# Optimization experiments

Measured on AMD Instinct MI355X. Metric: run time of the kernel, lower is better.

The kernel has to match this reference:

```python
import jax, jax.numpy as jnp
import numpy as np

BN_EPS = 1e-5

def _bn_relu(x, gamma, beta):
    # training-mode BatchNorm1d: biased batch stats over (B, N) per channel
    mean = x.mean(axis=(0, 2), keepdims=True)
    var = x.var(axis=(0, 2), keepdims=True)
    xn = (x - mean) * jax.lax.rsqrt(var + BN_EPS)
    return jax.nn.relu(xn * gamma[None, :, None] + beta[None, :, None])


def setup_inputs() -> dict:
    key = jax.random.key(0)
    ks = jax.random.split(key, 12)
    B, n1, n2, c1, c2 = 16, 4096, 1024, 128, 256
    in_ch, mlp = c1 + c2, [256, 128]
    xyz1 = jax.random.uniform(ks[0], (B, n1, 3), dtype=jnp.float32)
    xyz2 = jax.random.uniform(ks[1], (B, n2, 3), dtype=jnp.float32)
    feat1 = jax.random.normal(ks[2], (B, c1, n1), dtype=jnp.float32)
    feat2 = jax.random.normal(ks[3], (B, c2, n2), dtype=jnp.float32)
    # Conv1d(k=1) weights as (out, in) matrices; kaiming-ish scale
    w0 = jax.random.normal(ks[4], (mlp[0], in_ch), dtype=jnp.float32) / np.sqrt(in_ch)
    b0 = jnp.zeros((mlp[0],), jnp.float32)
    g0 = jnp.ones((mlp[0],), jnp.float32)
    be0 = jnp.zeros((mlp[0],), jnp.float32)
    w1 = jax.random.normal(ks[5], (mlp[1], mlp[0]), dtype=jnp.float32) / np.sqrt(mlp[0])
    b1 = jnp.zeros((mlp[1],), jnp.float32)
    g1 = jnp.ones((mlp[1],), jnp.float32)
    be1 = jnp.zeros((mlp[1],), jnp.float32)
    return {"xyz1": xyz1, "xyz2": xyz2, "feat1": feat1, "feat2": feat2,
            "w0": w0, "b0": b0, "g0": g0, "be0": be0,
            "w1": w1, "b1": b1, "g1": g1, "be1": be1}


def reference(xyz1, xyz2, feat1, feat2, w0, b0, g0, be0, w1, b1, g1, be1):
    # three_nn_interpolate: squared pairwise dists (B, n1, n2)
    d = jnp.sum((xyz1[:, :, None, :] - xyz2[:, None, :, :]) ** 2, axis=-1)
    neg_d3, idx3 = jax.lax.top_k(-d, 3)          # 3 smallest dists
    d3 = -neg_d3                                  # (B, n1, 3)
    w = 1.0 / (d3 + 1e-8)
    w = w / jnp.sum(w, axis=-1, keepdims=True)
    # gather feat2 at knn indices: (B, c2, n1, 3)
    gathered = jnp.take_along_axis(feat2[:, :, None, :], idx3[:, None, :, :], axis=3)
    interp = jnp.sum(gathered * w[:, None, :, :], axis=-1)  # (B, c2, n1)

    x = jnp.concatenate([feat1, interp], axis=1)            # (B, c1+c2, n1)
    x = _bn_relu(jnp.einsum('oc,bcn->bon', w0, x) + b0[None, :, None], g0, be0)
    x = _bn_relu(jnp.einsum('oc,bcn->bon', w1, x) + b1[None, :, None], g1, be1)
    return x
```

## Files before the change

### kernel.cpp

```cpp
#include <hip/hip_runtime.h>
#include <hip/hip_bf16.h>

typedef unsigned short u16;
typedef __attribute__((ext_vector_type(8))) __bf16 bf16x8;
typedef __attribute__((ext_vector_type(4))) float floatx4;

#define B_   16
#define N1_  4096
#define N2_  1024
#define C1_  128
#define C2_  256
#define CIN_ 384
#define CM_  256
#define CO_  128

__device__ __forceinline__ u16 f2bf(float f) {
  unsigned u = __float_as_uint(f);
  u = (u + 0x7fffu + ((u >> 16) & 1u)) >> 16;
  return (u16)u;
}
__device__ __forceinline__ float bf2f(u16 h) {
  return __uint_as_float(((unsigned)h) << 16);
}

union U128 { uint4 u; bf16x8 v; u16 s[8]; };

__device__ __forceinline__ bf16x8 ldfrag(const u16* p) {
  U128 x; x.u = *(const uint4*)p; return x.v;
}
__device__ __forceinline__ uint4 pack8(const u16* h) {
  uint4 u;
  u.x = (unsigned)h[0] | ((unsigned)h[1] << 16);
  u.y = (unsigned)h[2] | ((unsigned)h[3] << 16);
  u.z = (unsigned)h[4] | ((unsigned)h[5] << 16);
  u.w = (unsigned)h[6] | ((unsigned)h[7] << 16);
  return u;
}


__global__ __launch_bounds__(256) void knn_part_kernel(
    const float* __restrict__ xyz1, const float* __restrict__ xyz2,
    float* __restrict__ pd, int* __restrict__ pi,
    const float* __restrict__ w0, const float* __restrict__ w1,
    u16* __restrict__ w0b, u16* __restrict__ w1b)
{
  __shared__ float4 sp[128];
  int t = threadIdx.x;
  if (blockIdx.x == 16) {
    int item = (blockIdx.y * 8 + blockIdx.z) * 256 + t;
    if (item < 12288) {
      int m = item / 48, kc = item % 48;
      const float* p = w0 + m * CIN_ + kc * 8;
      u16 h8[8];
      #pragma unroll
      for (int j = 0; j < 8; ++j) h8[j] = f2bf(p[j]);
      int mt = m >> 4, col = m & 15, kt = kc >> 2, quad = kc & 3;
      *(uint4*)(w0b + ((mt*12 + kt)*512 + (quad*16 + col)*8)) = pack8(h8);
    } else if (item < 16384) {
      int i2 = item - 12288;
      int m = i2 >> 5, kc = i2 & 31;
      const float* p = w1 + m * CM_ + kc * 8;
      u16 h8[8];
      #pragma unroll
      for (int j = 0; j < 8; ++j) h8[j] = f2bf(p[j]);
      int mt = m >> 4, col = m & 15, kt = kc >> 2, quad = kc & 3;
      *(uint4*)(w1b + ((mt*8 + kt)*512 + (quad*16 + col)*8)) = pack8(h8);
    }
    return;
  }
  int b = blockIdx.y, chunk = blockIdx.z;
  const float* p2 = xyz2 + ((size_t)b * N2_ + chunk * 128) * 3;
  if (t < 128) sp[t] = make_float4(p2[t*3], p2[t*3+1], p2[t*3+2], 0.f);
  __syncthreads();
  int i = blockIdx.x * 256 + t;
  const float* p1 = xyz1 + ((size_t)b * N1_ + i) * 3;
  float x = p1[0], y = p1[1], z = p1[2];
  float d0 = 1e30f, d1 = 1e30f, d2 = 1e30f;
  int i0 = 0, i1 = 0, i2 = 0;
  int jb = chunk * 128;
  #pragma unroll 4
  for (int j = 0; j < 128; ++j) {
    float4 p = sp[j];
    float dx = x - p.x, dy = y - p.y, dz = z - p.z;
    float d = dx*dx + dy*dy + dz*dz;
    if (d < d2) {
      int jj = jb + j;
      if (d < d0)      { d2=d1; i2=i1; d1=d0; i1=i0; d0=d; i0=jj; }
      else if (d < d1) { d2=d1; i2=i1; d1=d;  i1=jj; }
      else             { d2=d;  i2=jj; }
    }
  }
  int o = chunk*65536 + b*4096 + i;
  pd[o] = d0; pd[o + 524288] = d1; pd[o + 1048576] = d2;
  pi[o] = i0; pi[o + 524288] = i1; pi[o + 1048576] = i2;
}

__global__ __launch_bounds__(256) void tr2m_kernel(
    const float* __restrict__ feat2, u16* __restrict__ feat2Tb,
    const float* __restrict__ pd, const int* __restrict__ pi,
    int* __restrict__ idx_out, float* __restrict__ w_out)
{
  __shared__ float sA[64][257];
  int t = threadIdx.x;
  if (blockIdx.x >= 16) {
    int p = (blockIdx.y * 16 + (blockIdx.x - 16)) * 256 + t;
    float d0 = 1e30f, d1 = 1e30f, d2 = 1e30f;
    int i0 = 0, i1 = 0, i2 = 0;
    #pragma unroll
    for (int c = 0; c < 8; ++c) {
      int o = c*65536 + p;
      #pragma unroll
      for (int k = 0; k < 3; ++k) {
        float d = pd[o + k*524288];
        int ix = pi[o + k*524288];
        bool c2 = d < d2, c1 = d < d1, c0 = d < d0;
        d2 = c1 ? d1 : (c2 ? d  : d2);
        i2 = c1 ? i1 : (c2 ? ix : i2);
        d1 = c0 ? d0 : (c1 ? d  : d1);
        i1 = c0 ? i0 : (c1 ? ix : i1);
        d0 = c0 ? d  : d0;
        i0 = c0 ? ix : i0;
      }
    }
    float w0 = 1.f/(d0+1e-8f), w1 = 1.f/(d1+1e-8f), w2 = 1.f/(d2+1e-8f);
    float inv = 1.f/(w0+w1+w2);
    idx_out[p]          = i0;
    idx_out[p +  65536] = i1;
    idx_out[p + 131072] = i2;
    w_out[p]            = w0*inv;
    w_out[p +  65536]   = w1*inv;
    w_out[p + 131072]   = w2*inv;
    return;
  }
  int b = blockIdx.y;
  int n0 = blockIdx.x * 64;
  #pragma unroll
  for (int j = 0; j < 16; ++j) {
    int flat4 = t + j * 256;
    int c = flat4 >> 4, nn4 = (flat4 & 15) * 4;
    float4 v = *(const float4*)(feat2 + ((size_t)b*C2_ + c)*N2_ + n0 + nn4);
    sA[nn4+0][c] = v.x; sA[nn4+1][c] = v.y; sA[nn4+2][c] = v.z; sA[nn4+3][c] = v.w;
  }
  __syncthreads();
  int nn = t & 63, chunk = t >> 6;
  u16* dst = feat2Tb + ((size_t)b*N2_ + n0 + nn)*C2_ + chunk*64;
  #pragma unroll
  for (int g = 0; g < 8; ++g) {
    u16 h8[8];
    #pragma unroll
    for (int j = 0; j < 8; ++j) h8[j] = f2bf(sA[nn][chunk*64 + g*8 + j]);
    *(uint4*)(dst + g*8) = pack8(h8);
  }
}

__global__ __launch_bounds__(256) void prep_fused_kernel(
    const float* __restrict__ feat1, const u16* __restrict__ feat2Tb,
    const int* __restrict__ idx_in, const float* __restrict__ w_in,
    u16* __restrict__ xcatT)
{
  __shared__ float sA[64][133];
  int b = blockIdx.y;
  int t = threadIdx.x;
  if (blockIdx.x < 64) {
    int n0 = blockIdx.x * 64;
    #pragma unroll
    for (int j = 0; j < 8; ++j) {
      int flat4 = t + j * 256;
      int c = flat4 >> 4, nn4 = (flat4 & 15) * 4;
      float4 v = *(const float4*)(feat1 + ((size_t)b*C1_ + c)*N1_ + n0 + nn4);
      sA[nn4+0][c] = v.x; sA[nn4+1][c] = v.y; sA[nn4+2][c] = v.z; sA[nn4+3][c] = v.w;
    }
    __syncthreads();
    int nn = t & 63, chunk = t >> 6;
    int n = n0 + nn, nt = n >> 4, col = n & 15;
    u16* tb = xcatT + ((size_t)b*256 + nt)*12*512;
    #pragma unroll
    for (int g = 0; g < 4; ++g) {
      int c0 = chunk*32 + g*8;
      u16 h8[8];
      #pragma unroll
      for (int j = 0; j < 8; ++j) h8[j] = f2bf(sA[nn][c0 + j]);
      *(uint4*)(tb + (size_t)chunk*512 + (g*16 + col)*8) = pack8(h8);
    }
  } else {
    int p0 = (blockIdx.x - 64) * 64;
    int seg = t & 31;
    int pl  = t >> 5;
    #pragma unroll 2
    for (int pass = 0; pass < 8; ++pass) {
      int n = p0 + pass*8 + pl;
      int base = b*N1_ + n;
      int i0 = idx_in[base], i1 = idx_in[base + 65536], i2 = idx_in[base + 131072];
      float w0 = w_in[base], w1 = w_in[base + 65536], w2 = w_in[base + 131072];
      const u16* fb = feat2Tb + (size_t)b*N2_*C2_ + seg*8;
      U128 a, c, d;
      a.u = *(const uint4*)(fb + (size_t)i0*C2_);
      c.u = *(const uint4*)(fb + (size_t)i1*C2_);
      d.u = *(const uint4*)(fb + (size_t)i2*C2_);
      u16 h8[8];
      #pragma unroll
      for (int j = 0; j < 8; ++j)
        h8[j] = f2bf(w0*bf2f(a.s[j]) + w1*bf2f(c.s[j]) + w2*bf2f(d.s[j]));
      int nt = n >> 4, col = n & 15;
      int kt = 4 + (seg >> 2), quad = seg & 3;
      *(uint4*)(xcatT + (((size_t)b*256 + nt)*12 + kt)*512 + (quad*16 + col)*8) = pack8(h8);
    }
  }
}

__global__ __launch_bounds__(256) void gemm1_mfma(
    const u16* __restrict__ xcatT, const u16* __restrict__ w0b,
    const float* __restrict__ b0p, u16* __restrict__ y0T,
    float* __restrict__ p0)
{
  __shared__ u16 sbuf[2][16][512];
  __shared__ float ps[4][64][2];
  int t = threadIdx.x;
  int wave = t >> 6, lane = t & 63;
  int col = lane & 15, quad = lane >> 4;
  int wm = wave >> 1, wn = wave & 1;
  int b = blockIdx.y;
  int mtb8 = blockIdx.z * 8;
  int ntb8 = blockIdx.x * 8;

  const u16* asrc = w0b + (size_t)mtb8 * 12 * 512 + lane * 8;
  const u16* bsrc = xcatT + ((size_t)(b * 256 + ntb8) * 12) * 512 + lane * 8;
  const u16* stage_base = (wave < 2) ? (asrc + (size_t)(wave * 4) * 12 * 512)
                                     : (bsrc + (size_t)((wave - 2) * 4) * 12 * 512);

  floatx4 acc[4][4] = {};

  #pragma unroll
  for (int i = 0; i < 4; ++i)
    __builtin_amdgcn_global_load_lds(
        (const __attribute__((address_space(1))) void*)(stage_base + (size_t)i * 12 * 512),
        (__attribute__((address_space(3))) void*)(&sbuf[0][wave * 4 + i][0]),
        16, 0, 0);
  __syncthreads();

  int cur = 0;
  #pragma unroll 1
  for (int kt = 0; kt < 12; ++kt) {
    if (kt < 11) {
      #pragma unroll
      for (int i = 0; i < 4; ++i)
        __builtin_amdgcn_global_load_lds(
            (const __attribute__((address_space(1))) void*)(stage_base + (size_t)(i * 12 + kt + 1) * 512),
            (__attribute__((address_space(3))) void*)(&sbuf[cur ^ 1][wave * 4 + i][0]),
            16, 0, 0);
    }
    bf16x8 af[4], bfr[4];
    #pragma unroll
    for (int i = 0; i < 4; ++i) {
      af[i]  = ldfrag(&sbuf[cur][wm * 4 + i][lane * 8]);
      bfr[i] = ldfrag(&sbuf[cur][8 + wn * 4 + i][lane * 8]);
    }
    #pragma unroll
    for (int mt = 0; mt < 4; ++mt)
      #pragma unroll
      for (int nt = 0; nt < 4; ++nt)
        acc[mt][nt] = __builtin_amdgcn_mfma_f32_16x16x32_bf16(af[mt], bfr[nt], acc[mt][nt], 0, 0, 0);
    __syncthreads();
    cur ^= 1;
  }

  int m0 = blockIdx.z*128 + wm*64;
  #pragma unroll
  for (int mt = 0; mt < 4; ++mt) {
    float4 bias4 = *(const float4*)(b0p + m0 + mt*16 + quad*4);
    float bia[4] = {bias4.x, bias4.y, bias4.z, bias4.w};
    int kt_out = (m0 >> 5) + (mt >> 1);
    int quad_out = ((mt & 1) << 1) | (quad >> 1);
    int j0 = (quad & 1) * 4;
    float s[4] = {}, q[4] = {};
    int ntb = ntb8 + wn*4;
    #pragma unroll
    for (int nt = 0; nt < 4; ++nt) {
      int nt_g = ntb + nt;
      u16 h[4];
      #pragma unroll
      for (int r = 0; r < 4; ++r) {
        float v = acc[mt][nt][r] + bia[r];
        u16 hh = f2bf(v);
        float vr = bf2f(hh);
        h[r] = hh; s[r] += vr; q[r] += vr*vr;
      }
      *(ushort4*)(y0T + (((size_t)b*256 + nt_g)*8 + kt_out)*512 + (quad_out*16 + col)*8 + j0)
          = make_ushort4(h[0], h[1], h[2], h[3]);
    }
    #pragma unroll
    for (int r = 0; r < 4; ++r) {
      float ss = s[r], qq = q[r];
      #pragma unroll
      for (int msk = 1; msk < 16; msk <<= 1) { ss += __shfl_xor(ss, msk); qq += __shfl_xor(qq, msk); }
      if (col == 0) {
        ps[wave][mt*16 + quad*4 + r][0] = ss;
        ps[wave][mt*16 + quad*4 + r][1] = qq;
      }
    }
  }
  __syncthreads();
  {
    int c = t >> 1, k = t & 1;
    int wbase = (c >> 6) * 2, ch = c & 63;
    float v = ps[wbase][ch][k] + ps[wbase+1][ch][k];
    size_t l = (size_t)blockIdx.z*512 + blockIdx.y*32 + blockIdx.x;
    p0[l*256 + t] = v;
  }
}

__global__ __launch_bounds__(256) void stats_kernel(
    const float* __restrict__ p, const float* __restrict__ g,
    const float* __restrict__ be, float* __restrict__ scale,
    float* __restrict__ shift, int half_split, int nl)
{
  int c = blockIdx.x, t = threadIdx.x;
  size_t base = half_split ? ((size_t)(c >> 7) * 512 * 256 + (size_t)(c & 127) * 2)
                           : ((size_t)c * 2);
  float s = 0.f, q = 0.f;
  for (int i = 0; i < nl; ++i) {
    float2 v = *(const float2*)(p + base + (size_t)(t + i*256) * 256);
    s += v.x; q += v.y;
  }
  #pragma unroll
  for (int m = 1; m < 64; m <<= 1) { s += __shfl_xor(s, m); q += __shfl_xor(q, m); }
  __shared__ float2 red[4];
  if ((t & 63) == 0) red[t >> 6] = make_float2(s, q);
  __syncthreads();
  if (t == 0) {
    float ss = red[0].x + red[1].x + red[2].x + red[3].x;
    float qq = red[0].y + red[1].y + red[2].y + red[3].y;
    float mu  = ss * (1.f/65536.f);
    float var = qq * (1.f/65536.f) - mu*mu;
    float a = g[c] * rsqrtf(var + 1e-5f);
    scale[c] = a; shift[c] = be[c] - mu*a;
  }
}

__global__ __launch_bounds__(256) void gemm2_mfma(
    const u16* __restrict__ y0T, const u16* __restrict__ w1b,
    const float* __restrict__ b1p,
    const float* __restrict__ scale0, const float* __restrict__ shift0,
    float* __restrict__ out, float* __restrict__ p1)
{
  __shared__ u16 sbuf[2][12][512];
  __shared__ float a0s[CM_], bb0s[CM_];
  __shared__ float ps[4][64][2];
  int t = threadIdx.x;
  a0s[t] = scale0[t]; bb0s[t] = shift0[t];
  int wave = t >> 6, lane = t & 63;
  int col = lane & 15, quad = lane >> 4;
  int wm = wave >> 1, wn = wave & 1;
  int b = blockIdx.y;
  int ntb4 = blockIdx.x * 4;

  const u16* src[3];
  #pragma unroll
  for (int i = 0; i < 3; ++i) {
    int f = wave * 3 + i;
    src[i] = (f < 8) ? (w1b + (size_t)(f * 8) * 512 + lane * 8)
                     : (y0T + ((size_t)(b * 256 + ntb4 + (f - 8)) * 8) * 512 + lane * 8);
  }

  floatx4 acc[4][2] = {};

  #pragma unroll
  for (int i = 0; i < 3; ++i)
    __builtin_amdgcn_global_load_lds(
        (const __attribute__((address_space(1))) void*)(src[i]),
        (__attribute__((address_space(3))) void*)(&sbuf[0][wave * 3 + i][0]),
        16, 0, 0);
  __syncthreads();

  int cur = 0;
  #pragma unroll 1
  for (int kt = 0; kt < 8; ++kt) {
    if (kt < 7) {
      #pragma unroll
      for (int i = 0; i < 3; ++i)
        __builtin_amdgcn_global_load_lds(
            (const __attribute__((address_space(1))) void*)(src[i] + (size_t)(kt + 1) * 512),
            (__attribute__((address_space(3))) void*)(&sbuf[cur ^ 1][wave * 3 + i][0]),
            16, 0, 0);
    }
    bf16x8 af[4]; U128 braw[2];
    #pragma unroll
    for (int i = 0; i < 4; ++i) af[i] = ldfrag(&sbuf[cur][wm * 4 + i][lane * 8]);
    #pragma unroll
    for (int j = 0; j < 2; ++j) braw[j].u = *(const uint4*)(&sbuf[cur][8 + wn * 2 + j][lane * 8]);
    int c0 = kt * 32 + quad * 8;
    float av[8], bv[8];
    *(float4*)&av[0] = *(const float4*)&a0s[c0];  *(float4*)&av[4] = *(const float4*)&a0s[c0+4];
    *(float4*)&bv[0] = *(const float4*)&bb0s[c0]; *(float4*)&bv[4] = *(const float4*)&bb0s[c0+4];
    bf16x8 bfv[2];
    #pragma unroll
    for (int j = 0; j < 2; ++j) {
      u16 h8[8];
      #pragma unroll
      for (int e = 0; e < 8; ++e)
        h8[e] = f2bf(fmaxf(fmaf(bf2f(braw[j].s[e]), av[e], bv[e]), 0.f));
      U128 x; x.u = pack8(h8); bfv[j] = x.v;
    }
    #pragma unroll
    for (int mt = 0; mt < 4; ++mt)
      #pragma unroll
      for (int nt = 0; nt < 2; ++nt)
        acc[mt][nt] = __builtin_amdgcn_mfma_f32_16x16x32_bf16(af[mt], bfv[nt], acc[mt][nt], 0, 0, 0);
    __syncthreads();
    cur ^= 1;
  }

  int m0 = wm * 64;
  int n0 = blockIdx.x * 64 + wn * 32;
  #pragma unroll
  for (int mt = 0; mt < 4; ++mt) {
    float4 bias4 = *(const float4*)(b1p + m0 + mt*16 + quad*4);
    float bia[4] = {bias4.x, bias4.y, bias4.z, bias4.w};
    float s[4] = {}, q[4] = {};
    #pragma unroll
    for (int nt = 0; nt < 2; ++nt) {
      int n = n0 + nt*16 + col;
      #pragma unroll
      for (int r = 0; r < 4; ++r) {
        float v = acc[mt][nt][r] + bia[r];
        out[((size_t)b*CO_ + m0 + mt*16 + quad*4 + r)*N1_ + n] = v;
        s[r] += v; q[r] += v*v;
      }
    }
    #pragma unroll
    for (int r = 0; r < 4; ++r) {
      float ss = s[r], qq = q[r];
      #pragma unroll
      for (int msk = 1; msk < 16; msk <<= 1) { ss += __shfl_xor(ss, msk); qq += __shfl_xor(qq, msk); }
      if (col == 0) {
        ps[wave][mt*16 + quad*4 + r][0] = ss;
        ps[wave][mt*16 + quad*4 + r][1] = qq;
      }
    }
  }
  __syncthreads();
  {
    int c = t >> 1, k = t & 1;
    int wbase = (c >> 6) * 2, ch = c & 63;
    float v = ps[wbase][ch][k] + ps[wbase+1][ch][k];
    size_t l = (size_t)blockIdx.y*64 + blockIdx.x;
    p1[l*256 + t] = v;
  }
}

__global__ __launch_bounds__(256) void bnrelu_kernel(
    float* __restrict__ out, const float* __restrict__ scale1, const float* __restrict__ shift1)
{
  int idx = blockIdx.x * 256 + threadIdx.x;
  int c = (idx >> 10) & (CO_ - 1);
  float a = scale1[c];
  float bb = shift1[c];
  float4 v = ((const float4*)out)[idx];
  v.x = fmaxf(fmaf(v.x, a, bb), 0.f);
  v.y = fmaxf(fmaf(v.y, a, bb), 0.f);
  v.z = fmaxf(fmaf(v.z, a, bb), 0.f);
  v.w = fmaxf(fmaf(v.w, a, bb), 0.f);
  ((float4*)out)[idx] = v;
}

extern "C" void kernel_launch(void* const* d_in, const int* in_sizes, int n_in,
                              void* d_out, int out_size, void* d_ws, size_t ws_size,
                              hipStream_t stream)
{
  const float* xyz1  = (const float*)d_in[0];
  const float* xyz2  = (const float*)d_in[1];
  const float* feat1 = (const float*)d_in[2];
  const float* feat2 = (const float*)d_in[3];
  const float* w0    = (const float*)d_in[4];
  const float* b0    = (const float*)d_in[5];
  const float* g0    = (const float*)d_in[6];
  const float* be0   = (const float*)d_in[7];
  const float* w1    = (const float*)d_in[8];
  const float* b1    = (const float*)d_in[9];
  const float* g1    = (const float*)d_in[10];
  const float* be1   = (const float*)d_in[11];
  float* out = (float*)d_out;
  char* ws = (char*)d_ws;

  u16*   xcatT   = (u16*)ws;
  float* knn_pd  = (float*)ws;
  float* p1      = (float*)ws;
  int*   knn_pi  = (int*)(ws + 6291456);
  u16*   y0T     = (u16*)(ws + 50331648);
  u16*   feat2Tb = (u16*)(ws + 50331648);
  u16*   w0b     = (u16*)(ws + 83886080);
  u16*   w1b     = (u16*)(ws + 84082688);
  int*   idx_buf = (int*)(ws + 84148224);
  float* w_buf   = (float*)(ws + 84934656);
  float* p0      = (float*)(ws + 85721088);
  float* scale0  = (float*)(ws + 87293952);
  float* shift0  = scale0 + 256;
  float* scale1  = scale0 + 512;
  float* shift1  = scale0 + 640;

  knn_part_kernel <<<dim3(17,16,8),   256, 0, stream>>>(xyz1, xyz2, knn_pd, knn_pi, w0, w1, w0b, w1b);
  tr2m_kernel     <<<dim3(32,16),     256, 0, stream>>>(feat2, feat2Tb, knn_pd, knn_pi, idx_buf, w_buf);
  prep_fused_kernel<<<dim3(128,16),   256, 0, stream>>>(feat1, feat2Tb, idx_buf, w_buf, xcatT);
  gemm1_mfma      <<<dim3(32,16,2),   256, 0, stream>>>(xcatT, w0b, b0, y0T, p0);
  stats_kernel    <<<256,             256, 0, stream>>>(p0, g0, be0, scale0, shift0, 1, 2);
  gemm2_mfma      <<<dim3(64,16),     256, 0, stream>>>(y0T, w1b, b1, scale0, shift0, out, p1);
  stats_kernel    <<<128,             256, 0, stream>>>(p1, g1, be1, scale1, shift1, 0, 4);
  bnrelu_kernel   <<<8192,            256, 0, stream>>>(out, scale1, shift1);
}
```

Before: 244.4 us.

## Use single-wave GEMM blocks with 128x64 tiles and channel-major stat partials

Both GEMM kernels drop from four-wave 256-thread blocks to single-wave 64-thread blocks. Each wave now computes an 8x4 grid of MFMA tiles and stages all A and B fragments itself, with no cross-wave LDS partial reduction. Per-block BN partial sums are written channel-major, so the stats kernel reads contiguous float2 values. This trades block-level cooperation for more independent blocks and higher per-wave register use. That may lower occupancy, and each wave now issues 12 global-to-LDS loads per k-step.

```diff
diff --git a/kernel.cpp b/kernel.cpp
--- a/kernel.cpp
+++ b/kernel.cpp
@@ -208,34 +208,33 @@
   }
 }
 
-__global__ __launch_bounds__(256) void gemm1_mfma(
+__global__ __launch_bounds__(64) void gemm1_mfma(
     const u16* __restrict__ xcatT, const u16* __restrict__ w0b,
     const float* __restrict__ b0p, u16* __restrict__ y0T,
     float* __restrict__ p0)
 {
-  __shared__ u16 sbuf[2][16][512];
-  __shared__ float ps[4][64][2];
-  int t = threadIdx.x;
-  int wave = t >> 6, lane = t & 63;
+  __shared__ u16 sbuf[2][12][512];
+  int lane = threadIdx.x;
   int col = lane & 15, quad = lane >> 4;
-  int wm = wave >> 1, wn = wave & 1;
-  int b = blockIdx.y;
-  int mtb8 = blockIdx.z * 8;
-  int ntb8 = blockIdx.x * 8;
-
-  const u16* asrc = w0b + (size_t)mtb8 * 12 * 512 + lane * 8;
-  const u16* bsrc = xcatT + ((size_t)(b * 256 + ntb8) * 12) * 512 + lane * 8;
-  const u16* stage_base = (wave < 2) ? (asrc + (size_t)(wave * 4) * 12 * 512)
-                                     : (bsrc + (size_t)((wave - 2) * 4) * 12 * 512);
-
-  floatx4 acc[4][4] = {};
-
-  #pragma unroll
-  for (int i = 0; i < 4; ++i)
+  int mb = blockIdx.x;
+  int gnb = blockIdx.y;
+  int b = gnb >> 6;
+  int ntb4 = (gnb & 63) * 4;
+
+  const u16* src[12];
+  #pragma unroll
+  for (int i = 0; i < 12; ++i)
+    src[i] = (i < 8)
+      ? (w0b + (size_t)((mb*8 + i) * 12) * 512 + lane*8)
+      : (xcatT + (size_t)((b*256 + ntb4 + (i-8)) * 12) * 512 + lane*8);
+
+  floatx4 acc[8][4] = {};
+
+  #pragma unroll
+  for (int i = 0; i < 12; ++i)
     __builtin_amdgcn_global_load_lds(
-        (const __attribute__((address_space(1))) void*)(stage_base + (size_t)i * 12 * 512),
-        (__attribute__((address_space(3))) void*)(&sbuf[0][wave * 4 + i][0]),
-        16, 0, 0);
+        (const __attribute__((address_space(1))) void*)(src[i]),
+        (__attribute__((address_space(3))) void*)(&sbuf[0][i][0]), 16, 0, 0);
   __syncthreads();
 
   int cur = 0;
@@ -243,20 +242,18 @@
   for (int kt = 0; kt < 12; ++kt) {
     if (kt < 11) {
       #pragma unroll
-      for (int i = 0; i < 4; ++i)
+      for (int i = 0; i < 12; ++i)
         __builtin_amdgcn_global_load_lds(
-            (const __attribute__((address_space(1))) void*)(stage_base + (size_t)(i * 12 + kt + 1) * 512),
-            (__attribute__((address_space(3))) void*)(&sbuf[cur ^ 1][wave * 4 + i][0]),
-            16, 0, 0);
-    }
-    bf16x8 af[4], bfr[4];
-    #pragma unroll
-    for (int i = 0; i < 4; ++i) {
-      af[i]  = ldfrag(&sbuf[cur][wm * 4 + i][lane * 8]);
-      bfr[i] = ldfrag(&sbuf[cur][8 + wn * 4 + i][lane * 8]);
-    }
-    #pragma unroll
-    for (int mt = 0; mt < 4; ++mt)
+            (const __attribute__((address_space(1))) void*)(src[i] + (size_t)(kt+1)*512),
+            (__attribute__((address_space(3))) void*)(&sbuf[cur^1][i][0]), 16, 0, 0);
+    }
+    bf16x8 af[8], bfr[4];
+    #pragma unroll
+    for (int i = 0; i < 8; ++i) af[i] = ldfrag(&sbuf[cur][i][lane*8]);
+    #pragma unroll
+    for (int j = 0; j < 4; ++j) bfr[j] = ldfrag(&sbuf[cur][8 + j][lane*8]);
+    #pragma unroll
+    for (int mt = 0; mt < 8; ++mt)
       #pragma unroll
       for (int nt = 0; nt < 4; ++nt)
         acc[mt][nt] = __builtin_amdgcn_mfma_f32_16x16x32_bf16(af[mt], bfr[nt], acc[mt][nt], 0, 0, 0);
@@ -264,19 +261,17 @@
     cur ^= 1;
   }
 
-  int m0 = blockIdx.z*128 + wm*64;
-  #pragma unroll
-  for (int mt = 0; mt < 4; ++mt) {
+  int m0 = mb * 128;
+  #pragma unroll
+  for (int mt = 0; mt < 8; ++mt) {
     float4 bias4 = *(const float4*)(b0p + m0 + mt*16 + quad*4);
     float bia[4] = {bias4.x, bias4.y, bias4.z, bias4.w};
-    int kt_out = (m0 >> 5) + (mt >> 1);
+    int kt_out = mb*4 + (mt >> 1);
     int quad_out = ((mt & 1) << 1) | (quad >> 1);
     int j0 = (quad & 1) * 4;
     float s[4] = {}, q[4] = {};
-    int ntb = ntb8 + wn*4;
     #pragma unroll
     for (int nt = 0; nt < 4; ++nt) {
-      int nt_g = ntb + nt;
       u16 h[4];
       #pragma unroll
       for (int r = 0; r < 4; ++r) {
@@ -285,7 +280,7 @@
         float vr = bf2f(hh);
         h[r] = hh; s[r] += vr; q[r] += vr*vr;
       }
-      *(ushort4*)(y0T + (((size_t)b*256 + nt_g)*8 + kt_out)*512 + (quad_out*16 + col)*8 + j0)
+      *(ushort4*)(y0T + (((size_t)b*256 + ntb4 + nt)*8 + kt_out)*512 + (quad_out*16 + col)*8 + j0)
           = make_ushort4(h[0], h[1], h[2], h[3]);
     }
     #pragma unroll
@@ -293,33 +288,24 @@
       float ss = s[r], qq = q[r];
       #pragma unroll
       for (int msk = 1; msk < 16; msk <<= 1) { ss += __shfl_xor(ss, msk); qq += __shfl_xor(qq, msk); }
-      if (col == 0) {
-        ps[wave][mt*16 + quad*4 + r][0] = ss;
-        ps[wave][mt*16 + quad*4 + r][1] = qq;
-      }
-    }
-  }
-  __syncthreads();
-  {
-    int c = t >> 1, k = t & 1;
-    int wbase = (c >> 6) * 2, ch = c & 63;
-    float v = ps[wbase][ch][k] + ps[wbase+1][ch][k];
-    size_t l = (size_t)blockIdx.z*512 + blockIdx.y*32 + blockIdx.x;
-    p0[l*256 + t] = v;
+      if (col == 0)
+        *(float2*)(p0 + ((size_t)(mb*128 + mt*16 + quad*4 + r) * 1024 + gnb) * 2)
+            = make_float2(ss, qq);
+    }
   }
 }
 
 __global__ __launch_bounds__(256) void stats_kernel(
     const float* __restrict__ p, const float* __restrict__ g,
     const float* __restrict__ be, float* __restrict__ scale,
-    float* __restrict__ shift, int half_split, int nl)
+    float* __restrict__ shift)
 {
   int c = blockIdx.x, t = threadIdx.x;
-  size_t base = half_split ? ((size_t)(c >> 7) * 512 * 256 + (size_t)(c & 127) * 2)
-                           : ((size_t)c * 2);
+  const float* base = p + (size_t)c * 2048;
   float s = 0.f, q = 0.f;
-  for (int i = 0; i < nl; ++i) {
-    float2 v = *(const float2*)(p + base + (size_t)(t + i*256) * 256);
+  #pragma unroll
+  for (int i = 0; i < 4; ++i) {
+    float2 v = *(const float2*)(base + (size_t)(t + i*256) * 2);
     s += v.x; q += v.y;
   }
   #pragma unroll
@@ -337,7 +323,7 @@
   }
 }
 
-__global__ __launch_bounds__(256) void gemm2_mfma(
+__global__ __launch_bounds__(64) void gemm2_mfma(
     const u16* __restrict__ y0T, const u16* __restrict__ w1b,
     const float* __restrict__ b1p,
     const float* __restrict__ scale0, const float* __restrict__ shift0,
@@ -345,31 +331,29 @@
 {
   __shared__ u16 sbuf[2][12][512];
   __shared__ float a0s[CM_], bb0s[CM_];
-  __shared__ float ps[4][64][2];
-  int t = threadIdx.x;
-  a0s[t] = scale0[t]; bb0s[t] = shift0[t];
-  int wave = t >> 6, lane = t & 63;
+  int lane = threadIdx.x;
   int col = lane & 15, quad = lane >> 4;
-  int wm = wave >> 1, wn = wave & 1;
-  int b = blockIdx.y;
-  int ntb4 = blockIdx.x * 4;
-
-  const u16* src[3];
-  #pragma unroll
-  for (int i = 0; i < 3; ++i) {
-    int f = wave * 3 + i;
-    src[i] = (f < 8) ? (w1b + (size_t)(f * 8) * 512 + lane * 8)
-                     : (y0T + ((size_t)(b * 256 + ntb4 + (f - 8)) * 8) * 512 + lane * 8);
-  }
-
-  floatx4 acc[4][2] = {};
-
-  #pragma unroll
-  for (int i = 0; i < 3; ++i)
+  int gnb = blockIdx.x;
+  int b = gnb >> 6;
+  int ntb4 = (gnb & 63) * 4;
+
+  *(float4*)&a0s[lane*4]  = *(const float4*)(scale0 + lane*4);
+  *(float4*)&bb0s[lane*4] = *(const float4*)(shift0 + lane*4);
+
+  const u16* src[12];
+  #pragma unroll
+  for (int i = 0; i < 12; ++i)
+    src[i] = (i < 8)
+      ? (w1b + (size_t)(i * 8) * 512 + lane*8)
+      : (y0T + (size_t)((b*256 + ntb4 + (i-8)) * 8) * 512 + lane*8);
+
+  floatx4 acc[8][4] = {};
+
+  #pragma unroll
+  for (int i = 0; i < 12; ++i)
     __builtin_amdgcn_global_load_lds(
         (const __attribute__((address_space(1))) void*)(src[i]),
-        (__attribute__((address_space(3))) void*)(&sbuf[0][wave * 3 + i][0]),
-        16, 0, 0);
+        (__attribute__((address_space(3))) void*)(&sbuf[0][i][0]), 16, 0, 0);
   __syncthreads();
 
   int cur = 0;
@@ -377,24 +361,23 @@
   for (int kt = 0; kt < 8; ++kt) {
     if (kt < 7) {
       #pragma unroll
-      for (int i = 0; i < 3; ++i)
+      for (int i = 0; i < 12; ++i)
         __builtin_amdgcn_global_load_lds(
-            (const __attribute__((address_space(1))) void*)(src[i] + (size_t)(kt + 1) * 512),
-            (__attribute__((address_space(3))) void*)(&sbuf[cur ^ 1][wave * 3 + i][0]),
-            16, 0, 0);
-    }
-    bf16x8 af[4]; U128 braw[2];
-    #pragma unroll
-    for (int i = 0; i < 4; ++i) af[i] = ldfrag(&sbuf[cur][wm * 4 + i][lane * 8]);
-    #pragma unroll
-    for (int j = 0; j < 2; ++j) braw[j].u = *(const uint4*)(&sbuf[cur][8 + wn * 2 + j][lane * 8]);
-    int c0 = kt * 32 + quad * 8;
+            (const __attribute__((address_space(1))) void*)(src[i] + (size_t)(kt+1)*512),
+            (__attribute__((address_space(3))) void*)(&sbuf[cur^1][i][0]), 16, 0, 0);
+    }
+    bf16x8 af[8]; U128 braw[4];
+    #pragma unroll
+    for (int i = 0; i < 8; ++i) af[i] = ldfrag(&sbuf[cur][i][lane*8]);
+    #pragma unroll
+    for (int j = 0; j < 4; ++j) braw[j].u = *(const uint4*)(&sbuf[cur][8 + j][lane*8]);
+    int c0 = kt*32 + quad*8;
     float av[8], bv[8];
     *(float4*)&av[0] = *(const float4*)&a0s[c0];  *(float4*)&av[4] = *(const float4*)&a0s[c0+4];
     *(float4*)&bv[0] = *(const float4*)&bb0s[c0]; *(float4*)&bv[4] = *(const float4*)&bb0s[c0+4];
-    bf16x8 bfv[2];
-    #pragma unroll
-    for (int j = 0; j < 2; ++j) {
+    bf16x8 bfv[4];
+    #pragma unroll
+    for (int j = 0; j < 4; ++j) {
       u16 h8[8];
       #pragma unroll
       for (int e = 0; e < 8; ++e)
@@ -402,28 +385,26 @@
       U128 x; x.u = pack8(h8); bfv[j] = x.v;
     }
     #pragma unroll
-    for (int mt = 0; mt < 4; ++mt)
-      #pragma unroll
-      for (int nt = 0; nt < 2; ++nt)
+    for (int mt = 0; mt < 8; ++mt)
+      #pragma unroll
+      for (int nt = 0; nt < 4; ++nt)
         acc[mt][nt] = __builtin_amdgcn_mfma_f32_16x16x32_bf16(af[mt], bfv[nt], acc[mt][nt], 0, 0, 0);
     __syncthreads();
     cur ^= 1;
   }
 
-  int m0 = wm * 64;
-  int n0 = blockIdx.x * 64 + wn * 32;
-  #pragma unroll
-  for (int mt = 0; mt < 4; ++mt) {
-    float4 bias4 = *(const float4*)(b1p + m0 + mt*16 + quad*4);
+  #pragma unroll
+  for (int mt = 0; mt < 8; ++mt) {
+    float4 bias4 = *(const float4*)(b1p + mt*16 + quad*4);
     float bia[4] = {bias4.x, bias4.y, bias4.z, bias4.w};
     float s[4] = {}, q[4] = {};
     #pragma unroll
-    for (int nt = 0; nt < 2; ++nt) {
-      int n = n0 + nt*16 + col;
+    for (int nt = 0; nt < 4; ++nt) {
+      int n = ntb4*16 + nt*16 + col;
       #pragma unroll
       for (int r = 0; r < 4; ++r) {
         float v = acc[mt][nt][r] + bia[r];
-        out[((size_t)b*CO_ + m0 + mt*16 + quad*4 + r)*N1_ + n] = v;
+        out[((size_t)b*CO_ + mt*16 + quad*4 + r)*N1_ + n] = v;
         s[r] += v; q[r] += v*v;
       }
     }
@@ -432,19 +413,10 @@
       float ss = s[r], qq = q[r];
       #pragma unroll
       for (int msk = 1; msk < 16; msk <<= 1) { ss += __shfl_xor(ss, msk); qq += __shfl_xor(qq, msk); }
-      if (col == 0) {
-        ps[wave][mt*16 + quad*4 + r][0] = ss;
-        ps[wave][mt*16 + quad*4 + r][1] = qq;
-      }
-    }
-  }
-  __syncthreads();
-  {
-    int c = t >> 1, k = t & 1;
-    int wbase = (c >> 6) * 2, ch = c & 63;
-    float v = ps[wbase][ch][k] + ps[wbase+1][ch][k];
-    size_t l = (size_t)blockIdx.y*64 + blockIdx.x;
-    p1[l*256 + t] = v;
+      if (col == 0)
+        *(float2*)(p1 + ((size_t)(mt*16 + quad*4 + r) * 1024 + gnb) * 2)
+            = make_float2(ss, qq);
+    }
   }
 }
 
@@ -492,7 +464,7 @@
   u16*   w1b     = (u16*)(ws + 84082688);
   int*   idx_buf = (int*)(ws + 84148224);
   float* w_buf   = (float*)(ws + 84934656);
-  float* p0      = (float*)(ws + 85721088);
+  float* p0      = (float*)(ws + 84148224);
   float* scale0  = (float*)(ws + 87293952);
   float* shift0  = scale0 + 256;
   float* scale1  = scale0 + 512;
@@ -501,9 +473,9 @@
   knn_part_kernel <<<dim3(17,16,8),   256, 0, stream>>>(xyz1, xyz2, knn_pd, knn_pi, w0, w1, w0b, w1b);
   tr2m_kernel     <<<dim3(32,16),     256, 0, stream>>>(feat2, feat2Tb, knn_pd, knn_pi, idx_buf, w_buf);
   prep_fused_kernel<<<dim3(128,16),   256, 0, stream>>>(feat1, feat2Tb, idx_buf, w_buf, xcatT);
-  gemm1_mfma      <<<dim3(32,16,2),   256, 0, stream>>>(xcatT, w0b, b0, y0T, p0);
-  stats_kernel    <<<256,             256, 0, stream>>>(p0, g0, be0, scale0, shift0, 1, 2);
-  gemm2_mfma      <<<dim3(64,16),     256, 0, stream>>>(y0T, w1b, b1, scale0, shift0, out, p1);
-  stats_kernel    <<<128,             256, 0, stream>>>(p1, g1, be1, scale1, shift1, 0, 4);
+  gemm1_mfma      <<<dim3(2,1024),     64, 0, stream>>>(xcatT, w0b, b0, y0T, p0);
+  stats_kernel    <<<256,             256, 0, stream>>>(p0, g0, be0, scale0, shift0);
+  gemm2_mfma      <<<1024,             64, 0, stream>>>(y0T, w1b, b1, scale0, shift0, out, p1);
+  stats_kernel    <<<128,             256, 0, stream>>>(p1, g1, be1, scale1, shift1);
   bnrelu_kernel   <<<8192,            256, 0, stream>>>(out, scale1, shift1);
 }
```

Result: slower. 256.5 us (+4.9%).

## Load GEMM fragments directly from global into registers with triple-buffered prefetch

Applied to the files above, without the earlier changes.

Both MFMA GEMM kernels drop the LDS double buffer filled by global_load_lds and the per-iteration barriers. Each wave now loads its own A and B fragments straight from global memory into registers, rotating three register buffers so loads run ahead of the MFMAs. gemm2 also doubles its N tile per block (half the grid) and adjusts the partial-stats indexing and stats_kernel argument to match. The cost is duplicated global or L2 traffic, since waves no longer share staged tiles, and higher register pressure.

```diff
diff --git a/kernel.cpp b/kernel.cpp
--- a/kernel.cpp
+++ b/kernel.cpp
@@ -213,56 +213,44 @@
     const float* __restrict__ b0p, u16* __restrict__ y0T,
     float* __restrict__ p0)
 {
-  __shared__ u16 sbuf[2][16][512];
   __shared__ float ps[4][64][2];
   int t = threadIdx.x;
   int wave = t >> 6, lane = t & 63;
   int col = lane & 15, quad = lane >> 4;
   int wm = wave >> 1, wn = wave & 1;
   int b = blockIdx.y;
-  int mtb8 = blockIdx.z * 8;
-  int ntb8 = blockIdx.x * 8;
-
-  const u16* asrc = w0b + (size_t)mtb8 * 12 * 512 + lane * 8;
-  const u16* bsrc = xcatT + ((size_t)(b * 256 + ntb8) * 12) * 512 + lane * 8;
-  const u16* stage_base = (wave < 2) ? (asrc + (size_t)(wave * 4) * 12 * 512)
-                                     : (bsrc + (size_t)((wave - 2) * 4) * 12 * 512);
+  int mtb = blockIdx.z*8 + wm*4;
+  int ntb = blockIdx.x*8 + wn*4;
+
+  const u16* ap = w0b + lane*8;
+  const u16* bp = xcatT + ((size_t)(b*256 + ntb)*12)*512 + lane*8;
 
   floatx4 acc[4][4] = {};
-
-  #pragma unroll
-  for (int i = 0; i < 4; ++i)
-    __builtin_amdgcn_global_load_lds(
-        (const __attribute__((address_space(1))) void*)(stage_base + (size_t)i * 12 * 512),
-        (__attribute__((address_space(3))) void*)(&sbuf[0][wave * 4 + i][0]),
-        16, 0, 0);
-  __syncthreads();
-
-  int cur = 0;
-  #pragma unroll 1
-  for (int kt = 0; kt < 12; ++kt) {
-    if (kt < 11) {
-      #pragma unroll
-      for (int i = 0; i < 4; ++i)
-        __builtin_amdgcn_global_load_lds(
-            (const __attribute__((address_space(1))) void*)(stage_base + (size_t)(i * 12 + kt + 1) * 512),
-            (__attribute__((address_space(3))) void*)(&sbuf[cur ^ 1][wave * 4 + i][0]),
-            16, 0, 0);
-    }
-    bf16x8 af[4], bfr[4];
-    #pragma unroll
-    for (int i = 0; i < 4; ++i) {
-      af[i]  = ldfrag(&sbuf[cur][wm * 4 + i][lane * 8]);
-      bfr[i] = ldfrag(&sbuf[cur][8 + wn * 4 + i][lane * 8]);
-    }
-    #pragma unroll
-    for (int mt = 0; mt < 4; ++mt)
-      #pragma unroll
-      for (int nt = 0; nt < 4; ++nt)
-        acc[mt][nt] = __builtin_amdgcn_mfma_f32_16x16x32_bf16(af[mt], bfr[nt], acc[mt][nt], 0, 0, 0);
-    __syncthreads();
-    cur ^= 1;
-  }
+  bf16x8 aA[4], aB[4], aC[4], bA[4], bB[4], bC[4];
+
+#define G1_LDA(BUF, KT) { _Pragma("unroll") for (int i = 0; i < 4; ++i) \
+    BUF[i] = ldfrag(ap + (size_t)((mtb+i)*12 + (KT))*512); }
+#define G1_LDB(BUF, KT) { _Pragma("unroll") for (int i = 0; i < 4; ++i) \
+    BUF[i] = ldfrag(bp + (size_t)(i*12 + (KT))*512); }
+#define G1_MM(A_, B_) { _Pragma("unroll") for (int mt = 0; mt < 4; ++mt) \
+    _Pragma("unroll") for (int nt = 0; nt < 4; ++nt) \
+      acc[mt][nt] = __builtin_amdgcn_mfma_f32_16x16x32_bf16(A_[mt], B_[nt], acc[mt][nt], 0, 0, 0); }
+
+  G1_LDA(aA,0);  G1_LDB(bA,0);
+  G1_LDA(aB,1);  G1_LDB(bB,1);
+  G1_LDA(aC,2);  G1_LDB(bC,2);
+  G1_MM(aA,bA);  G1_LDA(aA,3);  G1_LDB(bA,3);
+  G1_MM(aB,bB);  G1_LDA(aB,4);  G1_LDB(bB,4);
+  G1_MM(aC,bC);  G1_LDA(aC,5);  G1_LDB(bC,5);
+  G1_MM(aA,bA);  G1_LDA(aA,6);  G1_LDB(bA,6);
+  G1_MM(aB,bB);  G1_LDA(aB,7);  G1_LDB(bB,7);
+  G1_MM(aC,bC);  G1_LDA(aC,8);  G1_LDB(bC,8);
+  G1_MM(aA,bA);  G1_LDA(aA,9);  G1_LDB(bA,9);
+  G1_MM(aB,bB);  G1_LDA(aB,10); G1_LDB(bB,10);
+  G1_MM(aC,bC);  G1_LDA(aC,11); G1_LDB(bC,11);
+  G1_MM(aA,bA);
+  G1_MM(aB,bB);
+  G1_MM(aC,bC);
 
   int m0 = blockIdx.z*128 + wm*64;
   #pragma unroll
@@ -273,7 +261,6 @@
     int quad_out = ((mt & 1) << 1) | (quad >> 1);
     int j0 = (quad & 1) * 4;
     float s[4] = {}, q[4] = {};
-    int ntb = ntb8 + wn*4;
     #pragma unroll
     for (int nt = 0; nt < 4; ++nt) {
       int nt_g = ntb + nt;
@@ -343,82 +330,65 @@
     const float* __restrict__ scale0, const float* __restrict__ shift0,
     float* __restrict__ out, float* __restrict__ p1)
 {
-  __shared__ u16 sbuf[2][12][512];
   __shared__ float a0s[CM_], bb0s[CM_];
   __shared__ float ps[4][64][2];
   int t = threadIdx.x;
   a0s[t] = scale0[t]; bb0s[t] = shift0[t];
+  __syncthreads();
   int wave = t >> 6, lane = t & 63;
   int col = lane & 15, quad = lane >> 4;
   int wm = wave >> 1, wn = wave & 1;
   int b = blockIdx.y;
-  int ntb4 = blockIdx.x * 4;
-
-  const u16* src[3];
-  #pragma unroll
-  for (int i = 0; i < 3; ++i) {
-    int f = wave * 3 + i;
-    src[i] = (f < 8) ? (w1b + (size_t)(f * 8) * 512 + lane * 8)
-                     : (y0T + ((size_t)(b * 256 + ntb4 + (f - 8)) * 8) * 512 + lane * 8);
-  }
-
-  floatx4 acc[4][2] = {};
-
-  #pragma unroll
-  for (int i = 0; i < 3; ++i)
-    __builtin_amdgcn_global_load_lds(
-        (const __attribute__((address_space(1))) void*)(src[i]),
-        (__attribute__((address_space(3))) void*)(&sbuf[0][wave * 3 + i][0]),
-        16, 0, 0);
-  __syncthreads();
-
-  int cur = 0;
-  #pragma unroll 1
-  for (int kt = 0; kt < 8; ++kt) {
-    if (kt < 7) {
-      #pragma unroll
-      for (int i = 0; i < 3; ++i)
-        __builtin_amdgcn_global_load_lds(
-            (const __attribute__((address_space(1))) void*)(src[i] + (size_t)(kt + 1) * 512),
-            (__attribute__((address_space(3))) void*)(&sbuf[cur ^ 1][wave * 3 + i][0]),
-            16, 0, 0);
-    }
-    bf16x8 af[4]; U128 braw[2];
-    #pragma unroll
-    for (int i = 0; i < 4; ++i) af[i] = ldfrag(&sbuf[cur][wm * 4 + i][lane * 8]);
-    #pragma unroll
-    for (int j = 0; j < 2; ++j) braw[j].u = *(const uint4*)(&sbuf[cur][8 + wn * 2 + j][lane * 8]);
-    int c0 = kt * 32 + quad * 8;
-    float av[8], bv[8];
-    *(float4*)&av[0] = *(const float4*)&a0s[c0];  *(float4*)&av[4] = *(const float4*)&a0s[c0+4];
-    *(float4*)&bv[0] = *(const float4*)&bb0s[c0]; *(float4*)&bv[4] = *(const float4*)&bb0s[c0+4];
-    bf16x8 bfv[2];
-    #pragma unroll
-    for (int j = 0; j < 2; ++j) {
-      u16 h8[8];
-      #pragma unroll
-      for (int e = 0; e < 8; ++e)
-        h8[e] = f2bf(fmaxf(fmaf(bf2f(braw[j].s[e]), av[e], bv[e]), 0.f));
-      U128 x; x.u = pack8(h8); bfv[j] = x.v;
-    }
-    #pragma unroll
-    for (int mt = 0; mt < 4; ++mt)
-      #pragma unroll
-      for (int nt = 0; nt < 2; ++nt)
-        acc[mt][nt] = __builtin_amdgcn_mfma_f32_16x16x32_bf16(af[mt], bfv[nt], acc[mt][nt], 0, 0, 0);
-    __syncthreads();
-    cur ^= 1;
-  }
-
-  int m0 = wm * 64;
-  int n0 = blockIdx.x * 64 + wn * 32;
+  int mtb = wm*4;
+  int ntb = blockIdx.x*8 + wn*4;
+
+  const u16* ap = w1b + lane*8;
+  const u16* bp = y0T + ((size_t)(b*256 + ntb)*8)*512 + lane*8;
+
+  floatx4 acc[4][4] = {};
+  bf16x8 aA[4], aB[4], aC[4];
+  U128 rA[4], rB[4], rC[4];
+
+#define G2_LDA(BUF, KT) { _Pragma("unroll") for (int i = 0; i < 4; ++i) \
+    BUF[i] = ldfrag(ap + (size_t)((mtb+i)*8 + (KT))*512); }
+#define G2_LDB(BUF, KT) { _Pragma("unroll") for (int i = 0; i < 4; ++i) \
+    BUF[i].u = *(const uint4*)(bp + (size_t)(i*8 + (KT))*512); }
+#define G2_BNMM(A_, R_, KT) { \
+    int c0 = (KT)*32 + quad*8; \
+    float av[8], bv[8]; \
+    *(float4*)&av[0] = *(const float4*)&a0s[c0];  *(float4*)&av[4] = *(const float4*)&a0s[c0+4]; \
+    *(float4*)&bv[0] = *(const float4*)&bb0s[c0]; *(float4*)&bv[4] = *(const float4*)&bb0s[c0+4]; \
+    bf16x8 bfv[4]; \
+    _Pragma("unroll") for (int j = 0; j < 4; ++j) { \
+      u16 h8[8]; \
+      _Pragma("unroll") for (int e = 0; e < 8; ++e) \
+        h8[e] = f2bf(fmaxf(fmaf(bf2f(R_[j].s[e]), av[e], bv[e]), 0.f)); \
+      U128 x_; x_.u = pack8(h8); bfv[j] = x_.v; } \
+    _Pragma("unroll") for (int mt = 0; mt < 4; ++mt) \
+    _Pragma("unroll") for (int nt = 0; nt < 4; ++nt) \
+      acc[mt][nt] = __builtin_amdgcn_mfma_f32_16x16x32_bf16(A_[mt], bfv[nt], acc[mt][nt], 0, 0, 0); }
+
+  G2_LDA(aA,0);  G2_LDB(rA,0);
+  G2_LDA(aB,1);  G2_LDB(rB,1);
+  G2_LDA(aC,2);  G2_LDB(rC,2);
+  G2_BNMM(aA,rA,0);  G2_LDA(aA,3);  G2_LDB(rA,3);
+  G2_BNMM(aB,rB,1);  G2_LDA(aB,4);  G2_LDB(rB,4);
+  G2_BNMM(aC,rC,2);  G2_LDA(aC,5);  G2_LDB(rC,5);
+  G2_BNMM(aA,rA,3);  G2_LDA(aA,6);  G2_LDB(rA,6);
+  G2_BNMM(aB,rB,4);  G2_LDA(aB,7);  G2_LDB(rB,7);
+  G2_BNMM(aC,rC,5);
+  G2_BNMM(aA,rA,6);
+  G2_BNMM(aB,rB,7);
+
+  int m0 = wm*64;
+  int n0 = blockIdx.x*128 + wn*64;
   #pragma unroll
   for (int mt = 0; mt < 4; ++mt) {
     float4 bias4 = *(const float4*)(b1p + m0 + mt*16 + quad*4);
     float bia[4] = {bias4.x, bias4.y, bias4.z, bias4.w};
     float s[4] = {}, q[4] = {};
     #pragma unroll
-    for (int nt = 0; nt < 2; ++nt) {
+    for (int nt = 0; nt < 4; ++nt) {
       int n = n0 + nt*16 + col;
       #pragma unroll
       for (int r = 0; r < 4; ++r) {
@@ -443,7 +413,7 @@
     int c = t >> 1, k = t & 1;
     int wbase = (c >> 6) * 2, ch = c & 63;
     float v = ps[wbase][ch][k] + ps[wbase+1][ch][k];
-    size_t l = (size_t)blockIdx.y*64 + blockIdx.x;
+    size_t l = (size_t)blockIdx.y*32 + blockIdx.x;
     p1[l*256 + t] = v;
   }
 }
@@ -503,7 +473,7 @@
   prep_fused_kernel<<<dim3(128,16),   256, 0, stream>>>(feat1, feat2Tb, idx_buf, w_buf, xcatT);
   gemm1_mfma      <<<dim3(32,16,2),   256, 0, stream>>>(xcatT, w0b, b0, y0T, p0);
   stats_kernel    <<<256,             256, 0, stream>>>(p0, g0, be0, scale0, shift0, 1, 2);
-  gemm2_mfma      <<<dim3(64,16),     256, 0, stream>>>(y0T, w1b, b1, scale0, shift0, out, p1);
-  stats_kernel    <<<128,             256, 0, stream>>>(p1, g1, be1, scale1, shift1, 0, 4);
+  gemm2_mfma      <<<dim3(32,16),     256, 0, stream>>>(y0T, w1b, b1, scale0, shift0, out, p1);
+  stats_kernel    <<<128,             256, 0, stream>>>(p1, g1, be1, scale1, shift1, 0, 2);
   bnrelu_kernel   <<<8192,            256, 0, stream>>>(out, scale1, shift1);
 }
```

After: 252.0 us. 1.03x slower.

## Load gemm1 fragments directly to registers with triple buffering; fuse BN2 stats into apply

Applied to the files above, without the earlier changes.

gemm1 drops its LDS double-buffer staging and global_load_lds path. Each wave now loads its A and B MFMA fragments straight from global memory into registers, using a three-deep software pipeline that is fully unrolled over the 12 k-steps and has no barriers. Separately, the second-layer stats kernel and the BN+ReLU kernel are merged into one kernel. Each block reduces the partials for its channel and then applies the affine+ReLU. This removes a launch but repeats the partial reduction in every one of the 8 blocks per channel. The register approach raises VGPR pressure, and A tiles are now loaded redundantly by both waves sharing the same rows instead of being shared through LDS.

```diff
diff --git a/kernel.cpp b/kernel.cpp
--- a/kernel.cpp
+++ b/kernel.cpp
@@ -213,56 +213,44 @@
     const float* __restrict__ b0p, u16* __restrict__ y0T,
     float* __restrict__ p0)
 {
-  __shared__ u16 sbuf[2][16][512];
   __shared__ float ps[4][64][2];
   int t = threadIdx.x;
   int wave = t >> 6, lane = t & 63;
   int col = lane & 15, quad = lane >> 4;
   int wm = wave >> 1, wn = wave & 1;
   int b = blockIdx.y;
-  int mtb8 = blockIdx.z * 8;
-  int ntb8 = blockIdx.x * 8;
-
-  const u16* asrc = w0b + (size_t)mtb8 * 12 * 512 + lane * 8;
-  const u16* bsrc = xcatT + ((size_t)(b * 256 + ntb8) * 12) * 512 + lane * 8;
-  const u16* stage_base = (wave < 2) ? (asrc + (size_t)(wave * 4) * 12 * 512)
-                                     : (bsrc + (size_t)((wave - 2) * 4) * 12 * 512);
+  int mtb = blockIdx.z*8 + wm*4;
+  int ntb = blockIdx.x*8 + wn*4;
+
+  const u16* ap = w0b + lane*8;
+  const u16* bp = xcatT + ((size_t)(b*256 + ntb)*12)*512 + lane*8;
 
   floatx4 acc[4][4] = {};
-
-  #pragma unroll
-  for (int i = 0; i < 4; ++i)
-    __builtin_amdgcn_global_load_lds(
-        (const __attribute__((address_space(1))) void*)(stage_base + (size_t)i * 12 * 512),
-        (__attribute__((address_space(3))) void*)(&sbuf[0][wave * 4 + i][0]),
-        16, 0, 0);
-  __syncthreads();
-
-  int cur = 0;
-  #pragma unroll 1
-  for (int kt = 0; kt < 12; ++kt) {
-    if (kt < 11) {
-      #pragma unroll
-      for (int i = 0; i < 4; ++i)
-        __builtin_amdgcn_global_load_lds(
-            (const __attribute__((address_space(1))) void*)(stage_base + (size_t)(i * 12 + kt + 1) * 512),
-            (__attribute__((address_space(3))) void*)(&sbuf[cur ^ 1][wave * 4 + i][0]),
-            16, 0, 0);
-    }
-    bf16x8 af[4], bfr[4];
-    #pragma unroll
-    for (int i = 0; i < 4; ++i) {
-      af[i]  = ldfrag(&sbuf[cur][wm * 4 + i][lane * 8]);
-      bfr[i] = ldfrag(&sbuf[cur][8 + wn * 4 + i][lane * 8]);
-    }
-    #pragma unroll
-    for (int mt = 0; mt < 4; ++mt)
-      #pragma unroll
-      for (int nt = 0; nt < 4; ++nt)
-        acc[mt][nt] = __builtin_amdgcn_mfma_f32_16x16x32_bf16(af[mt], bfr[nt], acc[mt][nt], 0, 0, 0);
-    __syncthreads();
-    cur ^= 1;
-  }
+  bf16x8 aA[4], aB[4], aC[4], bA[4], bB[4], bC[4];
+
+#define G1_LDA(BUF, KT) { _Pragma("unroll") for (int i = 0; i < 4; ++i) \
+    BUF[i] = ldfrag(ap + (size_t)((mtb+i)*12 + (KT))*512); }
+#define G1_LDB(BUF, KT) { _Pragma("unroll") for (int i = 0; i < 4; ++i) \
+    BUF[i] = ldfrag(bp + (size_t)(i*12 + (KT))*512); }
+#define G1_MM(A_, B_) { _Pragma("unroll") for (int mt = 0; mt < 4; ++mt) \
+    _Pragma("unroll") for (int nt = 0; nt < 4; ++nt) \
+      acc[mt][nt] = __builtin_amdgcn_mfma_f32_16x16x32_bf16(A_[mt], B_[nt], acc[mt][nt], 0, 0, 0); }
+
+  G1_LDA(aA,0);  G1_LDB(bA,0);
+  G1_LDA(aB,1);  G1_LDB(bB,1);
+  G1_LDA(aC,2);  G1_LDB(bC,2);
+  G1_MM(aA,bA);  G1_LDA(aA,3);  G1_LDB(bA,3);
+  G1_MM(aB,bB);  G1_LDA(aB,4);  G1_LDB(bB,4);
+  G1_MM(aC,bC);  G1_LDA(aC,5);  G1_LDB(bC,5);
+  G1_MM(aA,bA);  G1_LDA(aA,6);  G1_LDB(bA,6);
+  G1_MM(aB,bB);  G1_LDA(aB,7);  G1_LDB(bB,7);
+  G1_MM(aC,bC);  G1_LDA(aC,8);  G1_LDB(bC,8);
+  G1_MM(aA,bA);  G1_LDA(aA,9);  G1_LDB(bA,9);
+  G1_MM(aB,bB);  G1_LDA(aB,10); G1_LDB(bB,10);
+  G1_MM(aC,bC);  G1_LDA(aC,11); G1_LDB(bC,11);
+  G1_MM(aA,bA);
+  G1_MM(aB,bB);
+  G1_MM(aC,bC);
 
   int m0 = blockIdx.z*128 + wm*64;
   #pragma unroll
@@ -273,7 +261,6 @@
     int quad_out = ((mt & 1) << 1) | (quad >> 1);
     int j0 = (quad & 1) * 4;
     float s[4] = {}, q[4] = {};
-    int ntb = ntb8 + wn*4;
     #pragma unroll
     for (int nt = 0; nt < 4; ++nt) {
       int nt_g = ntb + nt;
@@ -448,19 +435,46 @@
   }
 }
 
-__global__ __launch_bounds__(256) void bnrelu_kernel(
-    float* __restrict__ out, const float* __restrict__ scale1, const float* __restrict__ shift1)
-{
-  int idx = blockIdx.x * 256 + threadIdx.x;
-  int c = (idx >> 10) & (CO_ - 1);
-  float a = scale1[c];
-  float bb = shift1[c];
-  float4 v = ((const float4*)out)[idx];
-  v.x = fmaxf(fmaf(v.x, a, bb), 0.f);
-  v.y = fmaxf(fmaf(v.y, a, bb), 0.f);
-  v.z = fmaxf(fmaf(v.z, a, bb), 0.f);
-  v.w = fmaxf(fmaf(v.w, a, bb), 0.f);
-  ((float4*)out)[idx] = v;
+__global__ __launch_bounds__(256) void bnstats_kernel(
+    const float* __restrict__ p, const float* __restrict__ g,
+    const float* __restrict__ be, float* __restrict__ out)
+{
+  int c = blockIdx.y, t = threadIdx.x;
+  float s = 0.f, q = 0.f;
+  #pragma unroll
+  for (int i = 0; i < 4; ++i) {
+    float2 v = *(const float2*)(p + (size_t)(t + i*256) * 256 + c*2);
+    s += v.x; q += v.y;
+  }
+  #pragma unroll
+  for (int m = 1; m < 64; m <<= 1) { s += __shfl_xor(s, m); q += __shfl_xor(q, m); }
+  __shared__ float2 red[4];
+  __shared__ float ab[2];
+  if ((t & 63) == 0) red[t >> 6] = make_float2(s, q);
+  __syncthreads();
+  if (t == 0) {
+    float ss = red[0].x + red[1].x + red[2].x + red[3].x;
+    float qq = red[0].y + red[1].y + red[2].y + red[3].y;
+    float mu  = ss * (1.f/65536.f);
+    float var = qq * (1.f/65536.f) - mu*mu;
+    float a = g[c] * rsqrtf(var + 1e-5f);
+    ab[0] = a; ab[1] = be[c] - mu*a;
+  }
+  __syncthreads();
+  float a = ab[0], bb = ab[1];
+  int j0 = blockIdx.x * 2048;
+  #pragma unroll
+  for (int i = 0; i < 8; ++i) {
+    int j = j0 + t + i*256;
+    int b = j >> 10, n4 = j & 1023;
+    size_t fidx = ((size_t)(b * CO_ + c) << 10) + n4;
+    float4 v = ((const float4*)out)[fidx];
+    v.x = fmaxf(fmaf(v.x, a, bb), 0.f);
+    v.y = fmaxf(fmaf(v.y, a, bb), 0.f);
+    v.z = fmaxf(fmaf(v.z, a, bb), 0.f);
+    v.w = fmaxf(fmaf(v.w, a, bb), 0.f);
+    ((float4*)out)[fidx] = v;
+  }
 }
 
 extern "C" void kernel_launch(void* const* d_in, const int* in_sizes, int n_in,
@@ -495,8 +509,6 @@
   float* p0      = (float*)(ws + 85721088);
   float* scale0  = (float*)(ws + 87293952);
   float* shift0  = scale0 + 256;
-  float* scale1  = scale0 + 512;
-  float* shift1  = scale0 + 640;
 
   knn_part_kernel <<<dim3(17,16,8),   256, 0, stream>>>(xyz1, xyz2, knn_pd, knn_pi, w0, w1, w0b, w1b);
   tr2m_kernel     <<<dim3(32,16),     256, 0, stream>>>(feat2, feat2Tb, knn_pd, knn_pi, idx_buf, w_buf);
@@ -504,6 +516,5 @@
   gemm1_mfma      <<<dim3(32,16,2),   256, 0, stream>>>(xcatT, w0b, b0, y0T, p0);
   stats_kernel    <<<256,             256, 0, stream>>>(p0, g0, be0, scale0, shift0, 1, 2);
   gemm2_mfma      <<<dim3(64,16),     256, 0, stream>>>(y0T, w1b, b1, scale0, shift0, out, p1);
-  stats_kernel    <<<128,             256, 0, stream>>>(p1, g1, be1, scale1, shift1, 0, 4);
-  bnrelu_kernel   <<<8192,            256, 0, stream>>>(out, scale1, shift1);
-}
+  bnstats_kernel  <<<dim3(8,128),     256, 0, stream>>>(p1, g1, be1, out);
+}
```

Result: slower. 249.6 us (+2.1%).
